# Kernel optimization log

Measured on AMD Instinct MI355X. Metric: run time of the kernel, lower is better.

Reference implementation:

```python
import jax, jax.numpy as jnp
import numpy as np

WINDOW_SIZE = 11
SIGMA = 1.5
C1 = 0.01 ** 2
C2 = 0.03 ** 2


def _gaussian_window(window_size: int = WINDOW_SIZE, sigma: float = SIGMA) -> jnp.ndarray:
    x = np.arange(window_size)
    g = np.exp(-((x - window_size // 2) ** 2) / (2.0 * sigma ** 2)).astype(np.float32)
    g = g / g.sum()
    w2d = np.outer(g, g)  # [K, K]
    return jnp.asarray(w2d[None, None])  # [1, 1, K, K] (OIHW)


def _blur(x: jnp.ndarray, window: jnp.ndarray) -> jnp.ndarray:
    pad = WINDOW_SIZE // 2
    return jax.lax.conv_general_dilated(
        x, window, window_strides=(1, 1),
        padding=[(pad, pad), (pad, pad)],
        dimension_numbers=("NCHW", "OIHW", "NCHW"))


def setup_inputs() -> dict:
    key = jax.random.key(0)
    k1, k2 = jax.random.split(key)
    shape = (16, 1, 1024, 1024)
    img1 = jax.random.uniform(k1, shape, dtype=jnp.float32)
    img2 = jax.random.uniform(k2, shape, dtype=jnp.float32)
    return {"img1": img1, "img2": img2}


def reference(img1, img2) -> jnp.ndarray:
    window = _gaussian_window().astype(img1.dtype)
    mu1 = _blur(img1, window)
    mu2 = _blur(img2, window)
    mu1_sq = mu1 * mu1
    mu2_sq = mu2 * mu2
    mu1_mu2 = mu1 * mu2
    sigma1_sq = _blur(img1 * img1, window) - mu1_sq
    sigma2_sq = _blur(img2 * img2, window) - mu2_sq
    sigma12 = _blur(img1 * img2, window) - mu1_mu2
    ssim_map = ((2 * mu1_mu2 + C1) * (2 * sigma12 + C2)) / (
        (mu1_sq + mu2_sq + C1) * (sigma1_sq + sigma2_sq + C2))
    return 1.0 - ssim_map.mean()
```

## Files before the change

kernel.cpp:

```cpp
#include <hip/hip_runtime.h>
#include <hip/hip_fp16.h>

#define IMG_H 1024
#define IMG_W 1024
#define NIMG  16
#define RAD   5
#define KW    11
#define TX    64
#define STRIP 128
#define ASTEP 16
#define BSTEP 32
#define HBROWS (STRIP + 2*RAD)
#define RING  48
#define PADW  68
#define NQ    4
#define NPIX  (NIMG * IMG_H * IMG_W)

__device__ __forceinline__ float gw(int k) {
    constexpr float G[KW] = {
        0.00102838f, 0.00759876f, 0.03600077f, 0.10936070f, 0.21300554f,
        0.26601173f,
        0.21300554f, 0.10936070f, 0.03600077f, 0.00759876f, 0.00102838f};
    return G[k];
}

__device__ __forceinline__ unsigned h2u(__half2 v) {
    union { __half2 h; unsigned u; } c; c.h = v; return c.u;
}
__device__ __forceinline__ __half2 u2h(unsigned v) {
    union { unsigned u; __half2 h; } c; c.u = v; return c.h;
}
__device__ __forceinline__ __half2 hsel(const unsigned* hw, int idx) {
    unsigned r;
    if (idx & 1) r = (hw[idx >> 1] >> 16) | (hw[(idx >> 1) + 1] << 16);
    else         r = hw[idx >> 1];
    return u2h(r);
}

__global__ __launch_bounds__(256, 8) void ssim_strip_kernel(
        const float* __restrict__ img1, const float* __restrict__ img2,
        float* __restrict__ partial, int atomic_mode) {
    __shared__ __align__(16) __half hb[NQ][RING][PADW];
    __shared__ float wsum[4];

    const int t = threadIdx.x;
    const int tile_x = blockIdx.x * TX;
    const int tile_y = blockIdx.y * STRIP;
    const size_t img_off = (size_t)blockIdx.z * (IMG_H * IMG_W);
    const float* p1 = img1 + img_off;
    const float* p2 = img2 + img_off;

    const bool x_ok = (tile_x >= 8) && (tile_x + 72 <= IMG_W);

    auto phaseA = [&](int a) {
        const int tr = t >> 4;
        const int g4 = t & 15;
        const int h = ASTEP * a + tr;
        if (h >= HBROWS) return;
        int rr = h;
        if (rr >= 96) rr -= 96;
        else if (rr >= RING) rr -= RING;
        const int gr = tile_y + h - RAD;
        const int gc0 = tile_x + g4 * 4 - 8;
        const bool row_ok = (tile_y + ASTEP * a - RAD >= 0) &&
                            (tile_y + ASTEP * a + ASTEP - 1 - RAD < IMG_H);
        unsigned hwx[10], hwy[10];
        if (x_ok && row_ok) {
            const size_t base = (size_t)gr * IMG_W + gc0;
#pragma unroll
            for (int w = 0; w < 5; ++w) {
                const float4 xa = *reinterpret_cast<const float4*>(p1 + base + 4 * w);
                const float4 ya = *reinterpret_cast<const float4*>(p2 + base + 4 * w);
                hwx[2 * w]     = h2u(__floats2half2_rn(xa.x, xa.y));
                hwx[2 * w + 1] = h2u(__floats2half2_rn(xa.z, xa.w));
                hwy[2 * w]     = h2u(__floats2half2_rn(ya.x, ya.y));
                hwy[2 * w + 1] = h2u(__floats2half2_rn(ya.z, ya.w));
            }
        } else {
            const bool rowok = ((unsigned)gr < (unsigned)IMG_H);
            const float* row1 = p1 + (size_t)gr * IMG_W;
            const float* row2 = p2 + (size_t)gr * IMG_W;
#pragma unroll
            for (int w = 0; w < 5; ++w) {
                const int gc = gc0 + 4 * w;
                float4 xa = make_float4(0.f, 0.f, 0.f, 0.f);
                float4 ya = make_float4(0.f, 0.f, 0.f, 0.f);
                if (rowok) {
                    if (gc >= 0 && gc <= IMG_W - 4) {
                        xa = *reinterpret_cast<const float4*>(row1 + gc);
                        ya = *reinterpret_cast<const float4*>(row2 + gc);
                    } else if (gc > -4 && gc < IMG_W) {
                        float* ex = &xa.x;
                        float* ey = &ya.x;
#pragma unroll
                        for (int j = 0; j < 4; ++j) {
                            int g = gc + j;
                            if ((unsigned)g < (unsigned)IMG_W) {
                                ex[j] = row1[g];
                                ey[j] = row2[g];
                            }
                        }
                    }
                }
                hwx[2 * w]     = h2u(__floats2half2_rn(xa.x, xa.y));
                hwx[2 * w + 1] = h2u(__floats2half2_rn(xa.z, xa.w));
                hwy[2 * w]     = h2u(__floats2half2_rn(ya.x, ya.y));
                hwy[2 * w + 1] = h2u(__floats2half2_rn(ya.z, ya.w));
            }
        }
        __half2 A0[2], A1[2], A2[2], A3[2];
#pragma unroll
        for (int p = 0; p < 2; ++p)
            A0[p] = A1[p] = A2[p] = A3[p] = u2h(0u);
#pragma unroll
        for (int k = 0; k < KW; ++k) {
            const __half2 g2 = __float2half2_rn(gw(k));
#pragma unroll
            for (int p = 0; p < 2; ++p) {
                const int idx = 2 * p + 3 + k;
                const __half2 X = hsel(hwx, idx);
                const __half2 Y = hsel(hwy, idx);
                A0[p] = __hfma2(g2, X, A0[p]);
                A1[p] = __hfma2(g2, Y, A1[p]);
                const __half2 gx = __hmul2(g2, X);
                const __half2 gy = __hmul2(g2, Y);
                A2[p] = __hfma2(gx, X, A2[p]);
                A2[p] = __hfma2(gy, Y, A2[p]);
                A3[p] = __hfma2(gx, Y, A3[p]);
            }
        }
        *reinterpret_cast<uint2*>(&hb[0][rr][g4 * 4]) = make_uint2(h2u(A0[0]), h2u(A0[1]));
        *reinterpret_cast<uint2*>(&hb[1][rr][g4 * 4]) = make_uint2(h2u(A1[0]), h2u(A1[1]));
        *reinterpret_cast<uint2*>(&hb[2][rr][g4 * 4]) = make_uint2(h2u(A2[0]), h2u(A2[1]));
        *reinterpret_cast<uint2*>(&hb[3][rr][g4 * 4]) = make_uint2(h2u(A3[0]), h2u(A3[1]));
    };

    float lsum = 0.f;

    auto phaseB = [&](int s) {
        __half2 gh2[KW];
#pragma unroll
        for (int k = 0; k < KW; ++k) gh2[k] = __float2half2_rn(gw(k));

        const int rbase = (BSTEP * s) % RING;
        const int slot = t & 15;
        const int r2 = (t >> 4) * 2;
        __half2 acc[NQ][2][2];
#pragma unroll
        for (int q = 0; q < NQ; ++q)
#pragma unroll
            for (int rl = 0; rl < 2; ++rl)
#pragma unroll
                for (int cp = 0; cp < 2; ++cp)
                    acc[q][rl][cp] = u2h(0u);

#pragma unroll
        for (int q = 0; q < NQ; ++q) {
#pragma unroll
            for (int k = 0; k < KW + 1; ++k) {
                int r = rbase + r2 + k;
                if (r >= RING) r -= RING;
                const uint2 rv =
                    *reinterpret_cast<const uint2*>(&hb[q][r][slot * 4]);
                __half2 h0 = u2h(rv.x);
                __half2 h1 = u2h(rv.y);
                if (k < KW) {
                    acc[q][0][0] = __hfma2(gh2[k], h0, acc[q][0][0]);
                    acc[q][0][1] = __hfma2(gh2[k], h1, acc[q][0][1]);
                }
                if (k > 0) {
                    acc[q][1][0] = __hfma2(gh2[k - 1], h0, acc[q][1][0]);
                    acc[q][1][1] = __hfma2(gh2[k - 1], h1, acc[q][1][1]);
                }
            }
        }

        const float C1 = 0.0001f;
        const float C2 = 0.0009f;
#pragma unroll
        for (int rl = 0; rl < 2; ++rl) {
#pragma unroll
            for (int cp = 0; cp < 2; ++cp) {
                float2 m1p = __half22float2(acc[0][rl][cp]);
                float2 m2p = __half22float2(acc[1][rl][cp]);
                float2 Sp  = __half22float2(acc[2][rl][cp]);
                float2 Pp  = __half22float2(acc[3][rl][cp]);
#pragma unroll
                for (int e = 0; e < 2; ++e) {
                    float m1 = e ? m1p.y : m1p.x;
                    float m2 = e ? m2p.y : m2p.x;
                    float S  = e ? Sp.y  : Sp.x;
                    float P  = e ? Pp.y  : Pp.x;
                    float m1s = m1 * m1;
                    float m2s = m2 * m2;
                    float m12 = m1 * m2;
                    float sigsum = S - m1s - m2s;
                    float sig12  = P - m12;
                    float num = (2.f * m12 + C1) * (2.f * sig12 + C2);
                    float den = (m1s + m2s + C1) * (sigsum + C2);
                    lsum = fmaf(num, __builtin_amdgcn_rcpf(den), lsum);
                }
            }
        }
    };

#pragma unroll 1
    for (int a = 0; a < 9; ++a) {
        phaseA(a);
        __syncthreads();
        if (a >= 2 && ((a & 1) == 0)) {
            phaseB((a - 2) >> 1);
            __syncthreads();
        }
    }

#pragma unroll
    for (int off = 32; off > 0; off >>= 1)
        lsum += __shfl_down(lsum, off, 64);
    if ((t & 63) == 0) wsum[t >> 6] = lsum;
    __syncthreads();
    if (t == 0) {
        float s = wsum[0] + wsum[1] + wsum[2] + wsum[3];
        if (atomic_mode) {
            atomicAdd(partial, s);
        } else {
            int bid = (blockIdx.z * gridDim.y + blockIdx.y) * gridDim.x + blockIdx.x;
            partial[bid] = s;
        }
    }
}

__global__ __launch_bounds__(256) void ssim_reduce_kernel(
        const float* __restrict__ partial, int n, float* __restrict__ out) {
    float s = 0.f;
    for (int i = threadIdx.x; i < n; i += 256) s += partial[i];
#pragma unroll
    for (int off = 32; off > 0; off >>= 1)
        s += __shfl_down(s, off, 64);
    __shared__ float ws[4];
    if ((threadIdx.x & 63) == 0) ws[threadIdx.x >> 6] = s;
    __syncthreads();
    if (threadIdx.x == 0) {
        float tot = ws[0] + ws[1] + ws[2] + ws[3];
        out[0] = 1.f - tot / (float)NPIX;
    }
}

extern "C" void kernel_launch(void* const* d_in, const int* in_sizes, int n_in,
                              void* d_out, int out_size, void* d_ws, size_t ws_size,
                              hipStream_t stream) {
    const float* img1 = (const float*)d_in[0];
    const float* img2 = (const float*)d_in[1];
    float* out = (float*)d_out;
    float* partial = (float*)d_ws;

    dim3 grid(IMG_W / TX, IMG_H / STRIP, NIMG);
    const int nblocks = (IMG_W / TX) * (IMG_H / STRIP) * NIMG;
    const size_t needed = (size_t)nblocks * sizeof(float);

    if (ws_size >= needed) {
        ssim_strip_kernel<<<grid, 256, 0, stream>>>(img1, img2, partial, 0);
        ssim_reduce_kernel<<<1, 256, 0, stream>>>(partial, nblocks, out);
    } else {
        hipMemsetAsync(d_ws, 0, sizeof(float), stream);
        ssim_strip_kernel<<<grid, 256, 0, stream>>>(img1, img2, partial, 1);
        ssim_reduce_kernel<<<1, 256, 0, stream>>>(partial, 1, out);
    }
}
```

Before: 76.96 us.

## Give each wavefront a private column slice and LDS ring, dropping block barriers

Each 64-lane wavefront now owns a 16-column slice of the 64-wide tile and keeps its own horizontal-blur ring buffer in shared memory. With no data shared between wavefronts, the __syncthreads between the horizontal and vertical phases are removed. The intent is to let the four waves run independently and stop stalling on block-wide barriers. The cost is a slightly larger padded LDS footprint and a different bank-access pattern. Correctness now relies on intra-wave ordering of LDS writes and reads.

```diff
diff --git a/kernel.cpp b/kernel.cpp
--- a/kernel.cpp
+++ b/kernel.cpp
@@ -7,12 +7,13 @@
 #define RAD   5
 #define KW    11
 #define TX    64
+#define WTX   16
 #define STRIP 128
 #define ASTEP 16
 #define BSTEP 32
 #define HBROWS (STRIP + 2*RAD)
 #define RING  48
-#define PADW  68
+#define WPAD  20
 #define NQ    4
 #define NPIX  (NIMG * IMG_H * IMG_W)
 
@@ -40,28 +41,30 @@
 __global__ __launch_bounds__(256, 8) void ssim_strip_kernel(
         const float* __restrict__ img1, const float* __restrict__ img2,
         float* __restrict__ partial, int atomic_mode) {
-    __shared__ __align__(16) __half hb[NQ][RING][PADW];
+    __shared__ __align__(16) __half hb[4][NQ][RING][WPAD];
     __shared__ float wsum[4];
 
     const int t = threadIdx.x;
-    const int tile_x = blockIdx.x * TX;
+    const int wid = t >> 6;
+    const int lane = t & 63;
     const int tile_y = blockIdx.y * STRIP;
+    const int wx = blockIdx.x * TX + wid * WTX;
     const size_t img_off = (size_t)blockIdx.z * (IMG_H * IMG_W);
     const float* p1 = img1 + img_off;
     const float* p2 = img2 + img_off;
 
-    const bool x_ok = (tile_x >= 8) && (tile_x + 72 <= IMG_W);
+    const bool x_ok = (wx >= 8) && (wx + 24 <= IMG_W);
 
     auto phaseA = [&](int a) {
-        const int tr = t >> 4;
-        const int g4 = t & 15;
-        const int h = ASTEP * a + tr;
+        const int lr = lane >> 2;
+        const int g4 = lane & 3;
+        const int h = ASTEP * a + lr;
         if (h >= HBROWS) return;
         int rr = h;
         if (rr >= 96) rr -= 96;
         else if (rr >= RING) rr -= RING;
         const int gr = tile_y + h - RAD;
-        const int gc0 = tile_x + g4 * 4 - 8;
+        const int gc0 = wx + g4 * 4 - 8;
         const bool row_ok = (tile_y + ASTEP * a - RAD >= 0) &&
                             (tile_y + ASTEP * a + ASTEP - 1 - RAD < IMG_H);
         unsigned hwx[10], hwy[10];
@@ -129,10 +132,10 @@
                 A3[p] = __hfma2(gx, Y, A3[p]);
             }
         }
-        *reinterpret_cast<uint2*>(&hb[0][rr][g4 * 4]) = make_uint2(h2u(A0[0]), h2u(A0[1]));
-        *reinterpret_cast<uint2*>(&hb[1][rr][g4 * 4]) = make_uint2(h2u(A1[0]), h2u(A1[1]));
-        *reinterpret_cast<uint2*>(&hb[2][rr][g4 * 4]) = make_uint2(h2u(A2[0]), h2u(A2[1]));
-        *reinterpret_cast<uint2*>(&hb[3][rr][g4 * 4]) = make_uint2(h2u(A3[0]), h2u(A3[1]));
+        *reinterpret_cast<uint2*>(&hb[wid][0][rr][g4 * 4]) = make_uint2(h2u(A0[0]), h2u(A0[1]));
+        *reinterpret_cast<uint2*>(&hb[wid][1][rr][g4 * 4]) = make_uint2(h2u(A1[0]), h2u(A1[1]));
+        *reinterpret_cast<uint2*>(&hb[wid][2][rr][g4 * 4]) = make_uint2(h2u(A2[0]), h2u(A2[1]));
+        *reinterpret_cast<uint2*>(&hb[wid][3][rr][g4 * 4]) = make_uint2(h2u(A3[0]), h2u(A3[1]));
     };
 
     float lsum = 0.f;
@@ -143,8 +146,8 @@
         for (int k = 0; k < KW; ++k) gh2[k] = __float2half2_rn(gw(k));
 
         const int rbase = (BSTEP * s) % RING;
-        const int slot = t & 15;
-        const int r2 = (t >> 4) * 2;
+        const int slot = lane & 3;
+        const int r2 = (lane >> 2) * 2;
         __half2 acc[NQ][2][2];
 #pragma unroll
         for (int q = 0; q < NQ; ++q)
@@ -161,7 +164,7 @@
                 int r = rbase + r2 + k;
                 if (r >= RING) r -= RING;
                 const uint2 rv =
-                    *reinterpret_cast<const uint2*>(&hb[q][r][slot * 4]);
+                    *reinterpret_cast<const uint2*>(&hb[wid][q][r][slot * 4]);
                 __half2 h0 = u2h(rv.x);
                 __half2 h1 = u2h(rv.y);
                 if (k < KW) {
@@ -207,17 +210,15 @@
 #pragma unroll 1
     for (int a = 0; a < 9; ++a) {
         phaseA(a);
-        __syncthreads();
         if (a >= 2 && ((a & 1) == 0)) {
             phaseB((a - 2) >> 1);
-            __syncthreads();
         }
     }
 
 #pragma unroll
     for (int off = 32; off > 0; off >>= 1)
         lsum += __shfl_down(lsum, off, 64);
-    if ((t & 63) == 0) wsum[t >> 6] = lsum;
+    if (lane == 0) wsum[wid] = lsum;
     __syncthreads();
     if (t == 0) {
         float s = wsum[0] + wsum[1] + wsum[2] + wsum[3];
```

Result: faster. 67.68 us (median of 2 runs) (-12.1%).
